# Kernel optimization log

Measured on AMD Instinct MI355X. Metric: run time of the kernel, lower is better.

The kernel has to match this reference:

```python
import jax, jax.numpy as jnp
import numpy as np

EPS = 1e-5  # BatchNorm eps


def _unfold3x3(x):
    """torch.nn.Unfold(kernel=3, pad=1, stride=1) -> [B, H*W, 9, C] layout.

    Kernel positions are row-major (kh, kw); index 4 is the center, matching
    x_pn[:, :, 4:5, :] in the torch module.
    """
    B, C, H, W = x.shape
    xp = jnp.pad(x, ((0, 0), (0, 0), (1, 1), (1, 1)))
    patches = jnp.stack([xp[:, :, i:i + H, j:j + W]
                         for i in range(3) for j in range(3)], axis=1)  # [B,9,C,H,W]
    return patches.transpose(0, 3, 4, 1, 2).reshape(B, H * W, 9, C)


def setup_inputs() -> dict:
    key = jax.random.key(0)
    ks = jax.random.split(key, 10)
    B, Cin, Cout, H, W = 2, 64, 64, 64, 2048
    Ctot = 4 + Cin  # 4 meta channels + feature channels
    return {
        "x": jax.random.normal(ks[0], (B, Ctot, H, W), jnp.float32),
        "mask": jax.random.randint(ks[1], (B, 1, H, W), 0, 2, jnp.int32),
        # weight_mlp1: Linear(4 -> Cin, bias=False), torch layout [out, in]
        "W1": jax.random.normal(ks[2], (Cin, 4), jnp.float32) * 0.3,
        "bn1_g": jnp.ones((Cin,), jnp.float32),
        "bn1_b": jnp.zeros((Cin,), jnp.float32),
        "bn1_m": jax.random.normal(ks[3], (Cin,), jnp.float32) * 0.1,
        "bn1_v": jax.random.uniform(ks[4], (Cin,), jnp.float32, 0.5, 1.5),
        # weight_mlp2: Linear(Cin -> 1) (attention head)
        "W2": jax.random.normal(ks[5], (1, Cin), jnp.float32) * 0.1,
        "b2": jnp.zeros((1,), jnp.float32),
        # aggregation_mlp: Linear(9*Cin -> Cout, bias=False)
        "Wagg": jax.random.normal(ks[6], (Cout, 9 * Cin), jnp.float32) * 0.04,
        "bn2_g": jnp.ones((Cout,), jnp.float32),
        "bn2_b": jnp.zeros((Cout,), jnp.float32),
        "bn2_m": jax.random.normal(ks[7], (Cout,), jnp.float32) * 0.1,
        "bn2_v": jax.random.uniform(ks[8], (Cout,), jnp.float32, 0.5, 1.5),
    }


def reference(x, mask, W1, bn1_g, bn1_b, bn1_m, bn1_v, W2, b2,
              Wagg, bn2_g, bn2_b, bn2_m, bn2_v):
    B, Ctot, H, W_ = x.shape
    Cin = W1.shape[0]

    xu = _unfold3x3(x)                       # [B, HW, 9, Ctot]
    feats = xu[..., 4:]                      # [B, HW, 9, Cin]
    pn = xu[..., :4]                         # meta coords of 9 neighbors
    d = pn - pn[:, :, 4:5, :]                # relative to center pixel

    # per-neighbor weight MLP (Linear -> BN(eval) -> ReLU -> Linear)
    w = jnp.einsum('bnkm,cm->bnkc', d, W1)   # [B, HW, 9, Cin]
    w = (w - bn1_m) * (bn1_g * jax.lax.rsqrt(bn1_v + EPS)) + bn1_b
    w = jax.nn.relu(w)
    w = jnp.einsum('bnkc,oc->bnko', w, W2) + b2  # [B, HW, 9, 1]

    mu = _unfold3x3(mask.astype(jnp.float32))    # [B, HW, 9, 1]
    w = w * mu                                   # masked logits
    w = jax.nn.softmax(w[..., 0], axis=-1)[..., None]  # attention over 9 neighbors

    out = (w * feats).reshape(B, H * W_, 9 * Cin)
    y = jnp.einsum('bnf,of->bno', out, Wagg)     # [B, HW, Cout]
    y = (y - bn2_m) * (bn2_g * jax.lax.rsqrt(bn2_v + EPS)) + bn2_b
    y = jax.nn.relu(y)
    # Fold(kernel=1) == reshape back to the feature map
    return y.transpose(0, 2, 1).reshape(B, -1, H, W_)
```

## Files before the change

kernel.cpp:

```cpp
#include <hip/hip_runtime.h>
#include <hip/hip_bf16.h>

#define H_ 64
#define W_ 2048
#define HWsz (H_*W_)
#define CIN 64
#define CTOT 68
#define COUT 64

typedef float  f32x2  __attribute__((ext_vector_type(2)));
typedef float  f32x4  __attribute__((ext_vector_type(4)));
typedef float  f32x16 __attribute__((ext_vector_type(16)));
typedef short  s16x8  __attribute__((ext_vector_type(8)));

__device__ __forceinline__ unsigned short f2bf(float f) {
    unsigned u = __builtin_bit_cast(unsigned, f);
    unsigned r = u + 0x7fffu + ((u >> 16) & 1u);
    return (unsigned short)(r >> 16);
}

__device__ __forceinline__ unsigned pack2bf(float a, float b) {
    __hip_bfloat162 h = __float22bfloat162_rn(float2{a, b});
    unsigned u;
    __builtin_memcpy(&u, &h, 4);
    return u;
}

__global__ __launch_bounds__(256) void prep_bw(
    const float* __restrict__ Wagg,
    const float* __restrict__ W1, const float* __restrict__ g1,
    const float* __restrict__ b1, const float* __restrict__ m1,
    const float* __restrict__ v1, const float* __restrict__ W2,
    unsigned short* __restrict__ BwS, float* __restrict__ Wfold)
{
    int tid = threadIdx.x;
    if (blockIdx.x == 0) {
        if (tid < 64) {
            float s1 = g1[tid] * rsqrtf(v1[tid] + 1e-5f);
#pragma unroll
            for (int m = 0; m < 4; ++m) Wfold[tid*8 + m] = W1[tid*4 + m] * s1;
            Wfold[tid*8 + 4] = b1[tid] - m1[tid]*s1;
            Wfold[tid*8 + 5] = W2[tid];
            Wfold[tid*8 + 6] = 0.f;
            Wfold[tid*8 + 7] = 0.f;
        }
        __syncthreads();
        if (tid == 0) {
            float s = 0.f;
            for (int c = 0; c < 64; ++c) s += fmaxf(Wfold[c*8 + 4], 0.f) * Wfold[c*8 + 5];
            Wfold[512] = s;
        }
    }
    int idx = blockIdx.x * 256 + tid;
    if (idx < 4608) {
        int lane = idx & 63;
        int rest = idx >> 6;
        int nt = rest & 1;
        int ks = (rest >> 1) & 3;
        int k9 = rest >> 3;
        int o  = nt*32 + (lane & 31);
        int ch = ks*16 + (lane >> 5)*8;
        const float* src = Wagg + (size_t)o*(9*CIN) + k9*64 + ch;
        s16x8 v8;
#pragma unroll
        for (int j = 0; j < 8; ++j) v8[j] = (short)f2bf(src[j]);
        *(s16x8*)(BwS + (size_t)idx*8) = v8;
    }
}

__global__ __launch_bounds__(512, 8) void mega_k(
    const float* __restrict__ x, const int* __restrict__ mask,
    const unsigned short* __restrict__ BwS, const float* __restrict__ Wfold,
    const float* __restrict__ b2p,
    const float* __restrict__ g2, const float* __restrict__ bb2,
    const float* __restrict__ m2, const float* __restrict__ v2,
    float* __restrict__ out)
{
    __shared__ __align__(16) unsigned short fe[4][8][66][8];
    __shared__ __align__(16) float sw[2][9][64];
    __shared__ __align__(16) float sbn[2][64];

    const int tid = threadIdx.x;
    const int bx = blockIdx.x, by = blockIdx.y;
    const int b = by >> 5, h0 = (by & 31) << 1;
    const int w0 = bx << 6;
    const int lane = tid & 63, wv = tid >> 6;

    const float* xf = x + ((size_t)b*CTOT + 4)*HWsz;
    const float* xp = x + (size_t)b*CTOT*HWsz;
    const int*   mk = mask + (size_t)b*HWsz;

    if (tid >= 448) {
        int o = tid - 448;
        float sc = g2[o] * rsqrtf(v2[o] + 1e-5f);
        sbn[0][o] = sc;
        sbn[1][o] = bb2[o] - m2[o]*sc;
    }

#pragma unroll
    for (int r = 0; r < 4; ++r) {
        int gr = h0 - 1 + r;
        uint4 q = {0u, 0u, 0u, 0u};
        if ((unsigned)gr < (unsigned)H_) {
            const float* src = xf + (size_t)(wv*8)*HWsz + (size_t)gr*W_ + w0 + lane;
            float v[8];
#pragma unroll
            for (int j = 0; j < 8; ++j) v[j] = src[(size_t)j*HWsz];
            q.x = pack2bf(v[0], v[1]); q.y = pack2bf(v[2], v[3]);
            q.z = pack2bf(v[4], v[5]); q.w = pack2bf(v[6], v[7]);
        }
        *(uint4*)&fe[r][wv][1 + lane][0] = q;
    }
    if (tid < 64) {
        int c2 = tid & 1, g = (tid >> 1) & 7, r = tid >> 4;
        int gr = h0 - 1 + r, gc = w0 - 1 + c2*65;
        uint4 q = {0u, 0u, 0u, 0u};
        if (((unsigned)gr < (unsigned)H_) && ((unsigned)gc < (unsigned)W_)) {
            const float* src = xf + (size_t)(g*8)*HWsz + (size_t)gr*W_ + gc;
            float v[8];
#pragma unroll
            for (int j = 0; j < 8; ++j) v[j] = src[(size_t)j*HWsz];
            q.x = pack2bf(v[0], v[1]); q.y = pack2bf(v[2], v[3]);
            q.z = pack2bf(v[4], v[5]); q.w = pack2bf(v[6], v[7]);
        }
        *(uint4*)&fe[r][g][c2*65][0] = q;
    }

    const int px = tid & 63, gw = w0 + px;
    const int rowq = wv >> 2, tg = wv & 3;
    const int h = h0 + rowq;

    float pc[4];
#pragma unroll
    for (int ch = 0; ch < 4; ++ch) pc[ch] = xp[(size_t)ch*HWsz + (size_t)h*W_ + gw];

    const int ka = 2*tg + (tg >> 1);
    f32x2 dd[4]; f32x2 mu;
#pragma unroll
    for (int i = 0; i < 2; ++i) {
        int k = ka + i;
        int r = k/3 - 1, d = k%3 - 1;
        int ih = h + r, iw = gw + d;
        bool ok = ((unsigned)ih < (unsigned)H_) && ((unsigned)iw < (unsigned)W_);
        int ihc = min(max(ih, 0), H_-1);
        int iwc = min(max(iw, 0), W_-1);
        mu[i] = ok ? (float)mk[(size_t)ihc*W_ + iwc] : 0.f;
#pragma unroll
        for (int ch = 0; ch < 4; ++ch) {
            float p = xp[(size_t)ch*HWsz + (size_t)ihc*W_ + iwc];
            dd[ch][i] = (ok ? p : 0.f) - pc[ch];
        }
    }

    const f32x4* Wf4 = (const f32x4*)Wfold;
    const f32x2 z2 = {0.f, 0.f};
    f32x2 lg = z2;
#pragma unroll 8
    for (int c = 0; c < CIN; ++c) {
        f32x4 wa = Wf4[2*c];
        f32x4 wb = Wf4[2*c + 1];
        f32x2 v = {wb[0], wb[0]};
        v = dd[0]*wa[0] + v;
        v = dd[1]*wa[1] + v;
        v = dd[2]*wa[2] + v;
        v = dd[3]*wa[3] + v;
        v = __builtin_elementwise_max(v, z2);
        lg = v*wb[1] + lg;
    }
    float b2v = b2p[0];
    sw[rowq][ka    ][px] = (lg[0] + b2v) * mu[0];
    sw[rowq][ka + 1][px] = (lg[1] + b2v) * mu[1];
    __syncthreads();

    if (tid < 128) {
        int rq = tid >> 6, p2 = tid & 63;
        float mu4 = (float)mk[(size_t)(h0 + rq)*W_ + w0 + p2];
        float lgv[9];
#pragma unroll
        for (int k = 0; k < 9; ++k) if (k != 4) lgv[k] = sw[rq][k][p2];
        lgv[4] = (Wfold[512] + b2v) * mu4;
        float mx = -1e30f;
#pragma unroll
        for (int k = 0; k < 9; ++k) mx = fmaxf(mx, lgv[k]);
        float s = 0.f, e[9];
#pragma unroll
        for (int k = 0; k < 9; ++k) { e[k] = __expf(lgv[k] - mx); s += e[k]; }
        float inv = 1.f / s;
#pragma unroll
        for (int k = 0; k < 9; ++k) sw[rq][k][p2] = e[k] * inv;
    }
    __syncthreads();

    const int nt = wv & 1, rh = (wv >> 1) & 1, hv = wv >> 2;
    const int l31 = lane & 31, l5 = lane >> 5;
    const int hC = h0 + rh;

    const f32x16 fz16 = {0.f,0.f,0.f,0.f,0.f,0.f,0.f,0.f,0.f,0.f,0.f,0.f,0.f,0.f,0.f,0.f};
    f32x16 fin = fz16;

#pragma unroll
    for (int k9 = 0; k9 < 9; ++k9) {
        const int rr = rh + k9/3;
        const int dwp = k9 % 3;

        s16x8 aw[4];
#pragma unroll
        for (int ks = 0; ks < 4; ++ks)
            aw[ks] = *(const s16x8*)(BwS + (size_t)((((k9<<2) + ks)*2 + nt) << 9) + lane*8);

        const int col = hv*32 + l31 + dwp;
        f32x16 tmp = fz16;
#pragma unroll
        for (int ks = 0; ks < 4; ++ks) {
            s16x8 bfr = *(const s16x8*)&fe[rr][ks*2 + l5][col][0];
            tmp = __builtin_amdgcn_mfma_f32_32x32x16_bf16(aw[ks], bfr, tmp, 0, 0, 0);
        }
        float wsc = sw[rh][k9][hv*32 + l31];
#pragma unroll
        for (int c = 0; c < 16; ++c) fin[c] += wsc * tmp[c];
    }

    int obase = nt*32 + 4*l5;
    float* od = out + (((size_t)b*COUT + obase)*H_ + hC)*W_ + w0 + hv*32 + l31;
#pragma unroll
    for (int v = 0; v < 4; ++v) {
        f32x4 sc4 = *(const f32x4*)&sbn[0][obase + 8*v];
        f32x4 tc4 = *(const f32x4*)&sbn[1][obase + 8*v];
#pragma unroll
        for (int c = 0; c < 4; ++c)
            od[(size_t)(8*v + c)*HWsz] =
                fmaxf(fmaf(fin[4*v + c], sc4[c], tc4[c]), 0.f);
    }
}

extern "C" void kernel_launch(void* const* d_in, const int* in_sizes, int n_in,
                              void* d_out, int out_size, void* d_ws, size_t ws_size,
                              hipStream_t stream)
{
    const float* x    = (const float*)d_in[0];
    const int*   mask = (const int*)d_in[1];
    const float* W1   = (const float*)d_in[2];
    const float* g1   = (const float*)d_in[3];
    const float* b1   = (const float*)d_in[4];
    const float* m1   = (const float*)d_in[5];
    const float* v1   = (const float*)d_in[6];
    const float* W2   = (const float*)d_in[7];
    const float* b2   = (const float*)d_in[8];
    const float* Wagg = (const float*)d_in[9];
    const float* g2   = (const float*)d_in[10];
    const float* bb2  = (const float*)d_in[11];
    const float* m2   = (const float*)d_in[12];
    const float* v2   = (const float*)d_in[13];
    float* outp = (float*)d_out;

    char* ws = (char*)d_ws;
    unsigned short* BwS   = (unsigned short*)(ws + 0);
    float*          Wfold = (float*)(ws + 73728);

    hipLaunchKernelGGL(prep_bw, dim3(18), dim3(256), 0, stream,
                       Wagg, W1, g1, b1, m1, v1, W2, BwS, Wfold);
    hipLaunchKernelGGL(mega_k, dim3(W_/64, 64), dim3(512), 0, stream,
                       x, mask, BwS, Wfold, b2, g2, bb2, m2, v2, outp);
}
```

Before: 187.7 us.

## Make each block process four width tiles with double-buffered LDS staging

Each block now walks four consecutive 64-pixel tiles instead of one, keeping two LDS buffers for the feature halo and the attention weights. Global loads for the next tile are issued into registers while the current tile's MFMA aggregation and logit MLP run, so memory latency can overlap compute. The grid shrinks fourfold, LDS use doubles, occupancy hint drops from 8 to 4, and register pressure grows from the prefetch arrays.

```diff
diff --git a/kernel.cpp b/kernel.cpp
--- a/kernel.cpp
+++ b/kernel.cpp
@@ -7,6 +7,7 @@
 #define CIN 64
 #define CTOT 68
 #define COUT 64
+#define NT_ 4
 
 typedef float  f32x2  __attribute__((ext_vector_type(2)));
 typedef float  f32x4  __attribute__((ext_vector_type(4)));
@@ -68,7 +69,7 @@
     }
 }
 
-__global__ __launch_bounds__(512, 8) void mega_k(
+__global__ __launch_bounds__(512, 4) void mega_k(
     const float* __restrict__ x, const int* __restrict__ mask,
     const unsigned short* __restrict__ BwS, const float* __restrict__ Wfold,
     const float* __restrict__ b2p,
@@ -76,14 +77,14 @@
     const float* __restrict__ m2, const float* __restrict__ v2,
     float* __restrict__ out)
 {
-    __shared__ __align__(16) unsigned short fe[4][8][66][8];
-    __shared__ __align__(16) float sw[2][9][64];
+    __shared__ __align__(16) unsigned short fe[2][4][8][66][8];
+    __shared__ __align__(16) float sw[2][2][9][64];
     __shared__ __align__(16) float sbn[2][64];
 
     const int tid = threadIdx.x;
     const int bx = blockIdx.x, by = blockIdx.y;
     const int b = by >> 5, h0 = (by & 31) << 1;
-    const int w0 = bx << 6;
+    const int w00 = bx << 8;
     const int lane = tid & 63, wv = tid >> 6;
 
     const float* xf = x + ((size_t)b*CTOT + 4)*HWsz;
@@ -97,139 +98,187 @@
         sbn[1][o] = bb2[o] - m2[o]*sc;
     }
 
-#pragma unroll
-    for (int r = 0; r < 4; ++r) {
-        int gr = h0 - 1 + r;
-        uint4 q = {0u, 0u, 0u, 0u};
-        if ((unsigned)gr < (unsigned)H_) {
-            const float* src = xf + (size_t)(wv*8)*HWsz + (size_t)gr*W_ + w0 + lane;
-            float v[8];
-#pragma unroll
-            for (int j = 0; j < 8; ++j) v[j] = src[(size_t)j*HWsz];
-            q.x = pack2bf(v[0], v[1]); q.y = pack2bf(v[2], v[3]);
-            q.z = pack2bf(v[4], v[5]); q.w = pack2bf(v[6], v[7]);
-        }
-        *(uint4*)&fe[r][wv][1 + lane][0] = q;
-    }
-    if (tid < 64) {
-        int c2 = tid & 1, g = (tid >> 1) & 7, r = tid >> 4;
-        int gr = h0 - 1 + r, gc = w0 - 1 + c2*65;
-        uint4 q = {0u, 0u, 0u, 0u};
-        if (((unsigned)gr < (unsigned)H_) && ((unsigned)gc < (unsigned)W_)) {
-            const float* src = xf + (size_t)(g*8)*HWsz + (size_t)gr*W_ + gc;
-            float v[8];
-#pragma unroll
-            for (int j = 0; j < 8; ++j) v[j] = src[(size_t)j*HWsz];
-            q.x = pack2bf(v[0], v[1]); q.y = pack2bf(v[2], v[3]);
-            q.z = pack2bf(v[4], v[5]); q.w = pack2bf(v[6], v[7]);
-        }
-        *(uint4*)&fe[r][g][c2*65][0] = q;
-    }
-
-    const int px = tid & 63, gw = w0 + px;
+    const int px = tid & 63;
     const int rowq = wv >> 2, tg = wv & 3;
     const int h = h0 + rowq;
-
-    float pc[4];
-#pragma unroll
-    for (int ch = 0; ch < 4; ++ch) pc[ch] = xp[(size_t)ch*HWsz + (size_t)h*W_ + gw];
-
     const int ka = 2*tg + (tg >> 1);
-    f32x2 dd[4]; f32x2 mu;
-#pragma unroll
-    for (int i = 0; i < 2; ++i) {
-        int k = ka + i;
-        int r = k/3 - 1, d = k%3 - 1;
-        int ih = h + r, iw = gw + d;
-        bool ok = ((unsigned)ih < (unsigned)H_) && ((unsigned)iw < (unsigned)W_);
-        int ihc = min(max(ih, 0), H_-1);
-        int iwc = min(max(iw, 0), W_-1);
-        mu[i] = ok ? (float)mk[(size_t)ihc*W_ + iwc] : 0.f;
-#pragma unroll
-        for (int ch = 0; ch < 4; ++ch) {
-            float p = xp[(size_t)ch*HWsz + (size_t)ihc*W_ + iwc];
-            dd[ch][i] = (ok ? p : 0.f) - pc[ch];
-        }
-    }
-
-    const f32x4* Wf4 = (const f32x4*)Wfold;
-    const f32x2 z2 = {0.f, 0.f};
-    f32x2 lg = z2;
+
+    float pre[4][8];
+    float preh[4];
+    float pcv[4], rawp[2][4], rawm[2];
+
+    auto stage_load = [&](int w0t) {
+#pragma unroll
+        for (int r = 0; r < 4; ++r) {
+            int gr = h0 - 1 + r;
+            if ((unsigned)gr < (unsigned)H_) {
+                const float* src = xf + (size_t)(wv*8)*HWsz + (size_t)gr*W_ + w0t + lane;
+#pragma unroll
+                for (int j = 0; j < 8; ++j) pre[r][j] = src[(size_t)j*HWsz];
+            } else {
+#pragma unroll
+                for (int j = 0; j < 8; ++j) pre[r][j] = 0.f;
+            }
+        }
+        if (tid < 128) {
+            int c2 = tid & 1, jh = (tid >> 1) & 1, g = (tid >> 2) & 7, r = (tid >> 5) & 3;
+            int gr = h0 - 1 + r, gc = w0t - 1 + c2*65;
+            bool ok = ((unsigned)gr < (unsigned)H_) && ((unsigned)gc < (unsigned)W_);
+            int grc = min(max(gr, 0), H_-1), gcc = min(max(gc, 0), W_-1);
+            const float* src = xf + (size_t)(g*8 + jh*4)*HWsz + (size_t)grc*W_ + gcc;
+#pragma unroll
+            for (int j = 0; j < 4; ++j) preh[j] = ok ? src[(size_t)j*HWsz] : 0.f;
+        }
+    };
+
+    auto stage_write = [&](int tb) {
+#pragma unroll
+        for (int r = 0; r < 4; ++r) {
+            uint4 q;
+            q.x = pack2bf(pre[r][0], pre[r][1]); q.y = pack2bf(pre[r][2], pre[r][3]);
+            q.z = pack2bf(pre[r][4], pre[r][5]); q.w = pack2bf(pre[r][6], pre[r][7]);
+            *(uint4*)&fe[tb][r][wv][1 + lane][0] = q;
+        }
+        if (tid < 128) {
+            int c2 = tid & 1, jh = (tid >> 1) & 1, g = (tid >> 2) & 7, r = (tid >> 5) & 3;
+            uint2 q;
+            q.x = pack2bf(preh[0], preh[1]); q.y = pack2bf(preh[2], preh[3]);
+            *(uint2*)&fe[tb][r][g][c2*65][jh*4] = q;
+        }
+    };
+
+    auto logits_load = [&](int w0t) {
+        int gwt = w0t + px;
+#pragma unroll
+        for (int ch = 0; ch < 4; ++ch)
+            pcv[ch] = xp[(size_t)ch*HWsz + (size_t)h*W_ + gwt];
+#pragma unroll
+        for (int i = 0; i < 2; ++i) {
+            int k = ka + i;
+            int r = k/3 - 1, d = k%3 - 1;
+            int ih = h + r, iw = gwt + d;
+            bool ok = ((unsigned)ih < (unsigned)H_) && ((unsigned)iw < (unsigned)W_);
+            int ihc = min(max(ih, 0), H_-1);
+            int iwc = min(max(iw, 0), W_-1);
+            rawm[i] = ok ? (float)mk[(size_t)ihc*W_ + iwc] : 0.f;
+#pragma unroll
+            for (int ch = 0; ch < 4; ++ch) {
+                float p = xp[(size_t)ch*HWsz + (size_t)ihc*W_ + iwc];
+                rawp[i][ch] = ok ? p : 0.f;
+            }
+        }
+    };
+
+    auto logit_compute = [&](int tb, float b2v) {
+        f32x2 dd[4], mu;
+#pragma unroll
+        for (int i = 0; i < 2; ++i) {
+            mu[i] = rawm[i];
+#pragma unroll
+            for (int ch = 0; ch < 4; ++ch) dd[ch][i] = rawp[i][ch] - pcv[ch];
+        }
+        const f32x4* Wf4 = (const f32x4*)Wfold;
+        const f32x2 z2 = {0.f, 0.f};
+        f32x2 lg = z2;
 #pragma unroll 8
-    for (int c = 0; c < CIN; ++c) {
-        f32x4 wa = Wf4[2*c];
-        f32x4 wb = Wf4[2*c + 1];
-        f32x2 v = {wb[0], wb[0]};
-        v = dd[0]*wa[0] + v;
-        v = dd[1]*wa[1] + v;
-        v = dd[2]*wa[2] + v;
-        v = dd[3]*wa[3] + v;
-        v = __builtin_elementwise_max(v, z2);
-        lg = v*wb[1] + lg;
-    }
+        for (int c = 0; c < CIN; ++c) {
+            f32x4 wa = Wf4[2*c];
+            f32x4 wb = Wf4[2*c + 1];
+            f32x2 v = {wb[0], wb[0]};
+            v = dd[0]*wa[0] + v;
+            v = dd[1]*wa[1] + v;
+            v = dd[2]*wa[2] + v;
+            v = dd[3]*wa[3] + v;
+            v = __builtin_elementwise_max(v, z2);
+            lg = v*wb[1] + lg;
+        }
+        sw[tb][rowq][ka    ][px] = (lg[0] + b2v) * mu[0];
+        sw[tb][rowq][ka + 1][px] = (lg[1] + b2v) * mu[1];
+    };
+
+    auto softmax_ph = [&](int w0t, int tb, float ctr) {
+        if (tid < 128) {
+            int rq = tid >> 6, p2 = tid & 63;
+            float mu4 = (float)mk[(size_t)(h0 + rq)*W_ + w0t + p2];
+            float lgv[9];
+#pragma unroll
+            for (int k = 0; k < 9; ++k) if (k != 4) lgv[k] = sw[tb][rq][k][p2];
+            lgv[4] = ctr * mu4;
+            float mx = -1e30f;
+#pragma unroll
+            for (int k = 0; k < 9; ++k) mx = fmaxf(mx, lgv[k]);
+            float s = 0.f, e[9];
+#pragma unroll
+            for (int k = 0; k < 9; ++k) { e[k] = __expf(lgv[k] - mx); s += e[k]; }
+            float inv = 1.f / s;
+#pragma unroll
+            for (int k = 0; k < 9; ++k) sw[tb][rq][k][p2] = e[k] * inv;
+        }
+    };
+
+    auto phasec = [&](int w0t, int tb) {
+        const int nt = wv & 1, rh = (wv >> 1) & 1, hv = wv >> 2;
+        const int l31 = lane & 31, l5 = lane >> 5;
+        const int hC = h0 + rh;
+        const f32x16 fz16 = {0.f,0.f,0.f,0.f,0.f,0.f,0.f,0.f,
+                             0.f,0.f,0.f,0.f,0.f,0.f,0.f,0.f};
+        f32x16 fin = fz16;
+#pragma unroll
+        for (int k9 = 0; k9 < 9; ++k9) {
+            const int rr = rh + k9/3;
+            const int dwp = k9 % 3;
+            s16x8 aw[4];
+#pragma unroll
+            for (int ks = 0; ks < 4; ++ks)
+                aw[ks] = *(const s16x8*)(BwS + (size_t)((((k9<<2) + ks)*2 + nt) << 9) + lane*8);
+            const int col = hv*32 + l31 + dwp;
+            f32x16 tmp = fz16;
+#pragma unroll
+            for (int ks = 0; ks < 4; ++ks) {
+                s16x8 bfr = *(const s16x8*)&fe[tb][rr][ks*2 + l5][col][0];
+                tmp = __builtin_amdgcn_mfma_f32_32x32x16_bf16(aw[ks], bfr, tmp, 0, 0, 0);
+            }
+            float wsc = sw[tb][rh][k9][hv*32 + l31];
+#pragma unroll
+            for (int c = 0; c < 16; ++c) fin[c] += wsc * tmp[c];
+        }
+        int obase = nt*32 + 4*l5;
+        float* od = out + (((size_t)b*COUT + obase)*H_ + hC)*W_ + w0t + hv*32 + l31;
+#pragma unroll
+        for (int v = 0; v < 4; ++v) {
+            f32x4 sc4 = *(const f32x4*)&sbn[0][obase + 8*v];
+            f32x4 tc4 = *(const f32x4*)&sbn[1][obase + 8*v];
+#pragma unroll
+            for (int c = 0; c < 4; ++c)
+                od[(size_t)(8*v + c)*HWsz] =
+                    fmaxf(fmaf(fin[4*v + c], sc4[c], tc4[c]), 0.f);
+        }
+    };
+
     float b2v = b2p[0];
-    sw[rowq][ka    ][px] = (lg[0] + b2v) * mu[0];
-    sw[rowq][ka + 1][px] = (lg[1] + b2v) * mu[1];
+    float ctr = Wfold[512] + b2v;
+
+    stage_load(w00);
+    logits_load(w00);
+    stage_write(0);
+    stage_load(w00 + 64);
+    logit_compute(0, b2v);
     __syncthreads();
 
-    if (tid < 128) {
-        int rq = tid >> 6, p2 = tid & 63;
-        float mu4 = (float)mk[(size_t)(h0 + rq)*W_ + w0 + p2];
-        float lgv[9];
-#pragma unroll
-        for (int k = 0; k < 9; ++k) if (k != 4) lgv[k] = sw[rq][k][p2];
-        lgv[4] = (Wfold[512] + b2v) * mu4;
-        float mx = -1e30f;
-#pragma unroll
-        for (int k = 0; k < 9; ++k) mx = fmaxf(mx, lgv[k]);
-        float s = 0.f, e[9];
-#pragma unroll
-        for (int k = 0; k < 9; ++k) { e[k] = __expf(lgv[k] - mx); s += e[k]; }
-        float inv = 1.f / s;
-#pragma unroll
-        for (int k = 0; k < 9; ++k) sw[rq][k][p2] = e[k] * inv;
-    }
-    __syncthreads();
-
-    const int nt = wv & 1, rh = (wv >> 1) & 1, hv = wv >> 2;
-    const int l31 = lane & 31, l5 = lane >> 5;
-    const int hC = h0 + rh;
-
-    const f32x16 fz16 = {0.f,0.f,0.f,0.f,0.f,0.f,0.f,0.f,0.f,0.f,0.f,0.f,0.f,0.f,0.f,0.f};
-    f32x16 fin = fz16;
-
-#pragma unroll
-    for (int k9 = 0; k9 < 9; ++k9) {
-        const int rr = rh + k9/3;
-        const int dwp = k9 % 3;
-
-        s16x8 aw[4];
-#pragma unroll
-        for (int ks = 0; ks < 4; ++ks)
-            aw[ks] = *(const s16x8*)(BwS + (size_t)((((k9<<2) + ks)*2 + nt) << 9) + lane*8);
-
-        const int col = hv*32 + l31 + dwp;
-        f32x16 tmp = fz16;
-#pragma unroll
-        for (int ks = 0; ks < 4; ++ks) {
-            s16x8 bfr = *(const s16x8*)&fe[rr][ks*2 + l5][col][0];
-            tmp = __builtin_amdgcn_mfma_f32_32x32x16_bf16(aw[ks], bfr, tmp, 0, 0, 0);
-        }
-        float wsc = sw[rh][k9][hv*32 + l31];
-#pragma unroll
-        for (int c = 0; c < 16; ++c) fin[c] += wsc * tmp[c];
-    }
-
-    int obase = nt*32 + 4*l5;
-    float* od = out + (((size_t)b*COUT + obase)*H_ + hC)*W_ + w0 + hv*32 + l31;
-#pragma unroll
-    for (int v = 0; v < 4; ++v) {
-        f32x4 sc4 = *(const f32x4*)&sbn[0][obase + 8*v];
-        f32x4 tc4 = *(const f32x4*)&sbn[1][obase + 8*v];
-#pragma unroll
-        for (int c = 0; c < 4; ++c)
-            od[(size_t)(8*v + c)*HWsz] =
-                fmaxf(fmaf(fin[4*v + c], sc4[c], tc4[c]), 0.f);
+#pragma unroll
+    for (int t = 0; t < NT_; ++t) {
+        const int tb = t & 1;
+        const int w0t = w00 + t*64;
+        softmax_ph(w0t, tb, ctr);
+        __syncthreads();
+        phasec(w0t, tb);
+        if (t < NT_-1) {
+            logits_load(w0t + 64);
+            stage_write((t+1) & 1);
+            if (t < NT_-2) stage_load(w0t + 128);
+            logit_compute((t+1) & 1, b2v);
+            __syncthreads();
+        }
     }
 }
 
@@ -259,6 +308,6 @@
 
     hipLaunchKernelGGL(prep_bw, dim3(18), dim3(256), 0, stream,
                        Wagg, W1, g1, b1, m1, v1, W2, BwS, Wfold);
-    hipLaunchKernelGGL(mega_k, dim3(W_/64, 64), dim3(512), 0, stream,
+    hipLaunchKernelGGL(mega_k, dim3(W_/(64*NT_), 64), dim3(512), 0, stream,
                        x, mask, BwS, Wfold, b2, g2, bb2, m2, v2, outp);
 }
```

New measurement: 239.9 us. +27.8%, slower.

## Split fused kernel into softmax-weight kernel and MFMA aggregation kernel

Applied to the files above, without the earlier changes.

Splits the single fused kernel in two. The first computes the 9-neighbor softmax attention weights and writes them to a global workspace. The second loads the bf16 feature tile, reads those weights into registers, and runs the MFMA aggregation with 256-thread blocks where each wave covers both 32-pixel halves, reusing the A-fragments across them. This moves the attention-MLP latency out of the MFMA kernel and halves Wagg fragment loads per output, at the cost of an extra launch and a global round trip for about 9.4 MB of weights.

```diff
diff --git a/kernel.cpp b/kernel.cpp
--- a/kernel.cpp
+++ b/kernel.cpp
@@ -68,17 +68,12 @@
     }
 }
 
-__global__ __launch_bounds__(512, 8) void mega_k(
+__global__ __launch_bounds__(512, 8) void sw_k(
     const float* __restrict__ x, const int* __restrict__ mask,
-    const unsigned short* __restrict__ BwS, const float* __restrict__ Wfold,
-    const float* __restrict__ b2p,
-    const float* __restrict__ g2, const float* __restrict__ bb2,
-    const float* __restrict__ m2, const float* __restrict__ v2,
-    float* __restrict__ out)
-{
-    __shared__ __align__(16) unsigned short fe[4][8][66][8];
-    __shared__ __align__(16) float sw[2][9][64];
-    __shared__ __align__(16) float sbn[2][64];
+    const float* __restrict__ Wfold, const float* __restrict__ b2p,
+    float* __restrict__ sws)
+{
+    __shared__ float sw[2][9][64];
 
     const int tid = threadIdx.x;
     const int bx = blockIdx.x, by = blockIdx.y;
@@ -86,55 +81,18 @@
     const int w0 = bx << 6;
     const int lane = tid & 63, wv = tid >> 6;
 
-    const float* xf = x + ((size_t)b*CTOT + 4)*HWsz;
     const float* xp = x + (size_t)b*CTOT*HWsz;
     const int*   mk = mask + (size_t)b*HWsz;
 
-    if (tid >= 448) {
-        int o = tid - 448;
-        float sc = g2[o] * rsqrtf(v2[o] + 1e-5f);
-        sbn[0][o] = sc;
-        sbn[1][o] = bb2[o] - m2[o]*sc;
-    }
-
-#pragma unroll
-    for (int r = 0; r < 4; ++r) {
-        int gr = h0 - 1 + r;
-        uint4 q = {0u, 0u, 0u, 0u};
-        if ((unsigned)gr < (unsigned)H_) {
-            const float* src = xf + (size_t)(wv*8)*HWsz + (size_t)gr*W_ + w0 + lane;
-            float v[8];
-#pragma unroll
-            for (int j = 0; j < 8; ++j) v[j] = src[(size_t)j*HWsz];
-            q.x = pack2bf(v[0], v[1]); q.y = pack2bf(v[2], v[3]);
-            q.z = pack2bf(v[4], v[5]); q.w = pack2bf(v[6], v[7]);
-        }
-        *(uint4*)&fe[r][wv][1 + lane][0] = q;
-    }
-    if (tid < 64) {
-        int c2 = tid & 1, g = (tid >> 1) & 7, r = tid >> 4;
-        int gr = h0 - 1 + r, gc = w0 - 1 + c2*65;
-        uint4 q = {0u, 0u, 0u, 0u};
-        if (((unsigned)gr < (unsigned)H_) && ((unsigned)gc < (unsigned)W_)) {
-            const float* src = xf + (size_t)(g*8)*HWsz + (size_t)gr*W_ + gc;
-            float v[8];
-#pragma unroll
-            for (int j = 0; j < 8; ++j) v[j] = src[(size_t)j*HWsz];
-            q.x = pack2bf(v[0], v[1]); q.y = pack2bf(v[2], v[3]);
-            q.z = pack2bf(v[4], v[5]); q.w = pack2bf(v[6], v[7]);
-        }
-        *(uint4*)&fe[r][g][c2*65][0] = q;
-    }
-
-    const int px = tid & 63, gw = w0 + px;
+    const int px = lane, gw = w0 + px;
     const int rowq = wv >> 2, tg = wv & 3;
     const int h = h0 + rowq;
+    const int ka = 2*tg + (tg >> 1);
 
     float pc[4];
 #pragma unroll
     for (int ch = 0; ch < 4; ++ch) pc[ch] = xp[(size_t)ch*HWsz + (size_t)h*W_ + gw];
 
-    const int ka = 2*tg + (tg >> 1);
     f32x2 dd[4]; f32x2 mu;
 #pragma unroll
     for (int i = 0; i < 2; ++i) {
@@ -186,17 +144,83 @@
 #pragma unroll
         for (int k = 0; k < 9; ++k) { e[k] = __expf(lgv[k] - mx); s += e[k]; }
         float inv = 1.f / s;
-#pragma unroll
-        for (int k = 0; k < 9; ++k) sw[rq][k][p2] = e[k] * inv;
-    }
-    __syncthreads();
-
-    const int nt = wv & 1, rh = (wv >> 1) & 1, hv = wv >> 2;
+        float* dst = sws + ((size_t)(b*H_ + h0 + rq)*9)*W_ + w0 + p2;
+#pragma unroll
+        for (int k = 0; k < 9; ++k) dst[(size_t)k*W_] = e[k] * inv;
+    }
+}
+
+__global__ __launch_bounds__(256, 4) void agg_k(
+    const float* __restrict__ x, const float* __restrict__ sws,
+    const unsigned short* __restrict__ BwS,
+    const float* __restrict__ g2, const float* __restrict__ bb2,
+    const float* __restrict__ m2, const float* __restrict__ v2,
+    float* __restrict__ out)
+{
+    __shared__ __align__(16) unsigned short fe[4][8][66][8];
+    __shared__ __align__(16) float sbn[2][64];
+
+    const int tid = threadIdx.x;
+    const int bx = blockIdx.x, by = blockIdx.y;
+    const int b = by >> 5, h0 = (by & 31) << 1;
+    const int w0 = bx << 6;
+    const int lane = tid & 63, wv = tid >> 6;
+
+    const float* xf = x + ((size_t)b*CTOT + 4)*HWsz;
+
+    if (tid >= 192) {
+        int o = tid - 192;
+        float sc = g2[o] * rsqrtf(v2[o] + 1e-5f);
+        sbn[0][o] = sc;
+        sbn[1][o] = bb2[o] - m2[o]*sc;
+    }
+
+#pragma unroll
+    for (int it = 0; it < 8; ++it) {
+        int u = it*4 + wv;
+        int g = u & 7, r = u >> 3;
+        int gr = h0 - 1 + r;
+        uint4 q = {0u, 0u, 0u, 0u};
+        if ((unsigned)gr < (unsigned)H_) {
+            const float* src = xf + (size_t)(g*8)*HWsz + (size_t)gr*W_ + w0 + lane;
+            float v[8];
+#pragma unroll
+            for (int j = 0; j < 8; ++j) v[j] = src[(size_t)j*HWsz];
+            q.x = pack2bf(v[0], v[1]); q.y = pack2bf(v[2], v[3]);
+            q.z = pack2bf(v[4], v[5]); q.w = pack2bf(v[6], v[7]);
+        }
+        *(uint4*)&fe[r][g][1 + lane][0] = q;
+    }
+    if (tid < 64) {
+        int c2 = tid & 1, g = (tid >> 1) & 7, r = tid >> 4;
+        int gr = h0 - 1 + r, gc = w0 - 1 + c2*65;
+        uint4 q = {0u, 0u, 0u, 0u};
+        if (((unsigned)gr < (unsigned)H_) && ((unsigned)gc < (unsigned)W_)) {
+            const float* src = xf + (size_t)(g*8)*HWsz + (size_t)gr*W_ + gc;
+            float v[8];
+#pragma unroll
+            for (int j = 0; j < 8; ++j) v[j] = src[(size_t)j*HWsz];
+            q.x = pack2bf(v[0], v[1]); q.y = pack2bf(v[2], v[3]);
+            q.z = pack2bf(v[4], v[5]); q.w = pack2bf(v[6], v[7]);
+        }
+        *(uint4*)&fe[r][g][c2*65][0] = q;
+    }
+
+    const int nt = wv & 1, rh = wv >> 1;
     const int l31 = lane & 31, l5 = lane >> 5;
     const int hC = h0 + rh;
+    const float* swp = sws + ((size_t)(b*H_ + hC)*9)*W_ + w0 + l31;
+    float swr[2][9];
+#pragma unroll
+    for (int half = 0; half < 2; ++half)
+#pragma unroll
+        for (int k9 = 0; k9 < 9; ++k9)
+            swr[half][k9] = swp[(size_t)k9*W_ + half*32];
+
+    __syncthreads();
 
     const f32x16 fz16 = {0.f,0.f,0.f,0.f,0.f,0.f,0.f,0.f,0.f,0.f,0.f,0.f,0.f,0.f,0.f,0.f};
-    f32x16 fin = fz16;
+    f32x16 fin[2] = {fz16, fz16};
 
 #pragma unroll
     for (int k9 = 0; k9 < 9; ++k9) {
@@ -208,28 +232,34 @@
         for (int ks = 0; ks < 4; ++ks)
             aw[ks] = *(const s16x8*)(BwS + (size_t)((((k9<<2) + ks)*2 + nt) << 9) + lane*8);
 
-        const int col = hv*32 + l31 + dwp;
-        f32x16 tmp = fz16;
-#pragma unroll
-        for (int ks = 0; ks < 4; ++ks) {
-            s16x8 bfr = *(const s16x8*)&fe[rr][ks*2 + l5][col][0];
-            tmp = __builtin_amdgcn_mfma_f32_32x32x16_bf16(aw[ks], bfr, tmp, 0, 0, 0);
-        }
-        float wsc = sw[rh][k9][hv*32 + l31];
-#pragma unroll
-        for (int c = 0; c < 16; ++c) fin[c] += wsc * tmp[c];
+#pragma unroll
+        for (int half = 0; half < 2; ++half) {
+            int col = half*32 + l31 + dwp;
+            f32x16 tmp = fz16;
+#pragma unroll
+            for (int ks = 0; ks < 4; ++ks) {
+                s16x8 bfr = *(const s16x8*)&fe[rr][ks*2 + l5][col][0];
+                tmp = __builtin_amdgcn_mfma_f32_32x32x16_bf16(aw[ks], bfr, tmp, 0, 0, 0);
+            }
+            float wsc = swr[half][k9];
+#pragma unroll
+            for (int c = 0; c < 16; ++c) fin[half][c] += wsc * tmp[c];
+        }
     }
 
     int obase = nt*32 + 4*l5;
-    float* od = out + (((size_t)b*COUT + obase)*H_ + hC)*W_ + w0 + hv*32 + l31;
-#pragma unroll
-    for (int v = 0; v < 4; ++v) {
-        f32x4 sc4 = *(const f32x4*)&sbn[0][obase + 8*v];
-        f32x4 tc4 = *(const f32x4*)&sbn[1][obase + 8*v];
-#pragma unroll
-        for (int c = 0; c < 4; ++c)
-            od[(size_t)(8*v + c)*HWsz] =
-                fmaxf(fmaf(fin[4*v + c], sc4[c], tc4[c]), 0.f);
+#pragma unroll
+    for (int half = 0; half < 2; ++half) {
+        float* od = out + (((size_t)b*COUT + obase)*H_ + hC)*W_ + w0 + half*32 + l31;
+#pragma unroll
+        for (int v = 0; v < 4; ++v) {
+            f32x4 sc4 = *(const f32x4*)&sbn[0][obase + 8*v];
+            f32x4 tc4 = *(const f32x4*)&sbn[1][obase + 8*v];
+#pragma unroll
+            for (int c = 0; c < 4; ++c)
+                od[(size_t)(8*v + c)*HWsz] =
+                    fmaxf(fmaf(fin[half][4*v + c], sc4[c], tc4[c]), 0.f);
+        }
     }
 }
 
@@ -256,9 +286,12 @@
     char* ws = (char*)d_ws;
     unsigned short* BwS   = (unsigned short*)(ws + 0);
     float*          Wfold = (float*)(ws + 73728);
+    float*          sws   = (float*)(ws + 76800);
 
     hipLaunchKernelGGL(prep_bw, dim3(18), dim3(256), 0, stream,
                        Wagg, W1, g1, b1, m1, v1, W2, BwS, Wfold);
-    hipLaunchKernelGGL(mega_k, dim3(W_/64, 64), dim3(512), 0, stream,
-                       x, mask, BwS, Wfold, b2, g2, bb2, m2, v2, outp);
-}
+    hipLaunchKernelGGL(sw_k, dim3(W_/64, 64), dim3(512), 0, stream,
+                       x, mask, Wfold, b2, sws);
+    hipLaunchKernelGGL(agg_k, dim3(W_/64, 64), dim3(256), 0, stream,
+                       x, sws, BwS, g2, bb2, m2, v2, outp);
+}
```

Result: slower. 194.4 us (+3.5%).

## Stage position/mask halo in LDS, vectorize feature loads, prefetch MFMA weights

Applied to the files above, without the earlier changes.

Loads the 4 meta channels and the mask for the 4x66 halo tile into shared memory once, instead of having every thread issue scattered global gathers for its neighbours. Feature-tile loads now read two adjacent pixels per thread as float2, halving the load instruction count. MFMA weight fragments are double-buffered so the next k9 slice is fetched while the current one computes. Launch bounds drop to 4 blocks/SM, which allows more registers but may reduce occupancy, and an extra barrier plus some LDS is added.

```diff
diff --git a/kernel.cpp b/kernel.cpp
--- a/kernel.cpp
+++ b/kernel.cpp
@@ -68,7 +68,7 @@
     }
 }
 
-__global__ __launch_bounds__(512, 8) void mega_k(
+__global__ __launch_bounds__(512, 4) void mega_k(
     const float* __restrict__ x, const int* __restrict__ mask,
     const unsigned short* __restrict__ BwS, const float* __restrict__ Wfold,
     const float* __restrict__ b2p,
@@ -78,6 +78,8 @@
 {
     __shared__ __align__(16) unsigned short fe[4][8][66][8];
     __shared__ __align__(16) float sw[2][9][64];
+    __shared__ __align__(16) float posl[4][66][4];
+    __shared__ __align__(16) float mskl[4][66];
     __shared__ __align__(16) float sbn[2][64];
 
     const int tid = threadIdx.x;
@@ -90,26 +92,24 @@
     const float* xp = x + (size_t)b*CTOT*HWsz;
     const int*   mk = mask + (size_t)b*HWsz;
 
-    if (tid >= 448) {
-        int o = tid - 448;
-        float sc = g2[o] * rsqrtf(v2[o] + 1e-5f);
-        sbn[0][o] = sc;
-        sbn[1][o] = bb2[o] - m2[o]*sc;
-    }
-
-#pragma unroll
-    for (int r = 0; r < 4; ++r) {
+#pragma unroll
+    for (int cc = 0; cc < 2; ++cc) {
+        int task = tid + (cc << 9);
+        int px2 = task & 31, g = (task >> 5) & 7, r = task >> 8;
         int gr = h0 - 1 + r;
-        uint4 q = {0u, 0u, 0u, 0u};
+        uint4 q0 = {0u,0u,0u,0u}, q1 = {0u,0u,0u,0u};
         if ((unsigned)gr < (unsigned)H_) {
-            const float* src = xf + (size_t)(wv*8)*HWsz + (size_t)gr*W_ + w0 + lane;
-            float v[8];
-#pragma unroll
-            for (int j = 0; j < 8; ++j) v[j] = src[(size_t)j*HWsz];
-            q.x = pack2bf(v[0], v[1]); q.y = pack2bf(v[2], v[3]);
-            q.z = pack2bf(v[4], v[5]); q.w = pack2bf(v[6], v[7]);
-        }
-        *(uint4*)&fe[r][wv][1 + lane][0] = q;
+            const float* src = xf + (size_t)(g*8)*HWsz + (size_t)gr*W_ + w0 + 2*px2;
+            f32x2 v[8];
+#pragma unroll
+            for (int j = 0; j < 8; ++j) v[j] = *(const f32x2*)(src + (size_t)j*HWsz);
+            q0.x = pack2bf(v[0][0], v[1][0]); q0.y = pack2bf(v[2][0], v[3][0]);
+            q0.z = pack2bf(v[4][0], v[5][0]); q0.w = pack2bf(v[6][0], v[7][0]);
+            q1.x = pack2bf(v[0][1], v[1][1]); q1.y = pack2bf(v[2][1], v[3][1]);
+            q1.z = pack2bf(v[4][1], v[5][1]); q1.w = pack2bf(v[6][1], v[7][1]);
+        }
+        *(uint4*)&fe[r][g][1 + 2*px2][0] = q0;
+        *(uint4*)&fe[r][g][2 + 2*px2][0] = q1;
     }
     if (tid < 64) {
         int c2 = tid & 1, g = (tid >> 1) & 7, r = tid >> 4;
@@ -125,31 +125,45 @@
         }
         *(uint4*)&fe[r][g][c2*65][0] = q;
     }
-
-    const int px = tid & 63, gw = w0 + px;
+    if (tid >= 64 && tid < 64 + 264) {
+        int idx = tid - 64;
+        int r = idx / 66, col = idx - r*66;
+        int gr = h0 - 1 + r, gc = w0 - 1 + col;
+        bool ok = ((unsigned)gr < (unsigned)H_) && ((unsigned)gc < (unsigned)W_);
+        size_t off = (size_t)max(gr,0)*W_ + max(gc,0);
+        f32x4 p4 = {0.f, 0.f, 0.f, 0.f};
+        float mval = 0.f;
+        if (ok) {
+#pragma unroll
+            for (int ch = 0; ch < 4; ++ch) p4[ch] = xp[(size_t)ch*HWsz + off];
+            mval = (float)mk[off];
+        }
+        *(f32x4*)&posl[r][col][0] = p4;
+        mskl[r][col] = mval;
+    }
+    if (tid >= 448) {
+        int o = tid - 448;
+        float sc = g2[o] * rsqrtf(v2[o] + 1e-5f);
+        sbn[0][o] = sc;
+        sbn[1][o] = bb2[o] - m2[o]*sc;
+    }
+    __syncthreads();
+
+    const int px = lane;
     const int rowq = wv >> 2, tg = wv & 3;
-    const int h = h0 + rowq;
-
-    float pc[4];
-#pragma unroll
-    for (int ch = 0; ch < 4; ++ch) pc[ch] = xp[(size_t)ch*HWsz + (size_t)h*W_ + gw];
-
     const int ka = 2*tg + (tg >> 1);
+
+    f32x4 pcv = *(const f32x4*)&posl[rowq + 1][1 + px][0];
+
     f32x2 dd[4]; f32x2 mu;
 #pragma unroll
     for (int i = 0; i < 2; ++i) {
         int k = ka + i;
-        int r = k/3 - 1, d = k%3 - 1;
-        int ih = h + r, iw = gw + d;
-        bool ok = ((unsigned)ih < (unsigned)H_) && ((unsigned)iw < (unsigned)W_);
-        int ihc = min(max(ih, 0), H_-1);
-        int iwc = min(max(iw, 0), W_-1);
-        mu[i] = ok ? (float)mk[(size_t)ihc*W_ + iwc] : 0.f;
-#pragma unroll
-        for (int ch = 0; ch < 4; ++ch) {
-            float p = xp[(size_t)ch*HWsz + (size_t)ihc*W_ + iwc];
-            dd[ch][i] = (ok ? p : 0.f) - pc[ch];
-        }
+        int dr = k/3 - 1, dc = k%3 - 1;
+        f32x4 pv = *(const f32x4*)&posl[rowq + 1 + dr][1 + px + dc][0];
+        mu[i] = mskl[rowq + 1 + dr][1 + px + dc];
+#pragma unroll
+        for (int ch = 0; ch < 4; ++ch) dd[ch][i] = pv[ch] - pcv[ch];
     }
 
     const f32x4* Wf4 = (const f32x4*)Wfold;
@@ -174,7 +188,7 @@
 
     if (tid < 128) {
         int rq = tid >> 6, p2 = tid & 63;
-        float mu4 = (float)mk[(size_t)(h0 + rq)*W_ + w0 + p2];
+        float mu4 = mskl[rq + 1][1 + p2];
         float lgv[9];
 #pragma unroll
         for (int k = 0; k < 9; ++k) if (k != 4) lgv[k] = sw[rq][k][p2];
@@ -198,26 +212,31 @@
     const f32x16 fz16 = {0.f,0.f,0.f,0.f,0.f,0.f,0.f,0.f,0.f,0.f,0.f,0.f,0.f,0.f,0.f,0.f};
     f32x16 fin = fz16;
 
+    s16x8 awp[2][4];
+#pragma unroll
+    for (int ks = 0; ks < 4; ++ks)
+        awp[0][ks] = *(const s16x8*)(BwS + (size_t)((ks*2 + nt) << 9) + lane*8);
+
 #pragma unroll
     for (int k9 = 0; k9 < 9; ++k9) {
+        const int cb = k9 & 1;
+        if (k9 < 8) {
+#pragma unroll
+            for (int ks = 0; ks < 4; ++ks)
+                awp[cb ^ 1][ks] = *(const s16x8*)(BwS +
+                    (size_t)((((k9+1)*4 + ks)*2 + nt) << 9) + lane*8);
+        }
         const int rr = rh + k9/3;
         const int dwp = k9 % 3;
-
-        s16x8 aw[4];
-#pragma unroll
-        for (int ks = 0; ks < 4; ++ks)
-            aw[ks] = *(const s16x8*)(BwS + (size_t)((((k9<<2) + ks)*2 + nt) << 9) + lane*8);
-
         const int col = hv*32 + l31 + dwp;
         f32x16 tmp = fz16;
 #pragma unroll
         for (int ks = 0; ks < 4; ++ks) {
             s16x8 bfr = *(const s16x8*)&fe[rr][ks*2 + l5][col][0];
-            tmp = __builtin_amdgcn_mfma_f32_32x32x16_bf16(aw[ks], bfr, tmp, 0, 0, 0);
+            tmp = __builtin_amdgcn_mfma_f32_32x32x16_bf16(awp[cb][ks], bfr, tmp, 0, 0, 0);
         }
         float wsc = sw[rh][k9][hv*32 + l31];
-#pragma unroll
-        for (int c = 0; c < 16; ++c) fin[c] += wsc * tmp[c];
+        fin += tmp * wsc;
     }
 
     int obase = nt*32 + 4*l5;
```

Result: slower. 195.9 us (+4.3%).
